# Kernel tuning notes

Hardware: AMD Instinct MI355X
Metric: run time of the kernel (lower is better)

Reference implementation:

```python
import jax, jax.numpy as jnp
import numpy as np

L, N, E, H, D, F = 2048, 2, 1024, 16, 64, 4096  # seq, batch, embed, heads, head_dim, ffn
EPS = 1e-5


def _ln(x, w, b):
    m = jnp.mean(x, axis=-1, keepdims=True)
    v = jnp.mean(jnp.square(x - m), axis=-1, keepdims=True)
    return (x - m) * jax.lax.rsqrt(v + EPS) * w + b


def setup_inputs() -> dict:
    key = jax.random.key(0)
    ks = jax.random.split(key, 16)
    s = 0.02
    f32 = jnp.float32
    return {
        "x": jax.random.normal(ks[0], (L, N, E), f32),
        "ln1_w": jnp.ones((E,), f32),
        "ln1_b": jnp.zeros((E,), f32),
        "wq": jax.random.normal(ks[1], (H * D, E), f32) * s,
        "bq": jnp.zeros((H * D,), f32),
        "wk": jax.random.normal(ks[2], (H * D, E), f32) * s,
        "bk": jnp.zeros((H * D,), f32),
        "wv": jax.random.normal(ks[3], (H * D, E), f32) * s,
        "bv": jnp.zeros((H * D,), f32),
        "wout": jax.random.normal(ks[4], (E, H * D), f32) * s,
        "bout": jnp.zeros((E,), f32),
        "ln2_w": jnp.ones((E,), f32),
        "ln2_b": jnp.zeros((E,), f32),
        "fc1_w": jax.random.normal(ks[5], (F, E), f32) * s,
        "fc1_b": jnp.zeros((F,), f32),
        "fc2_w": jax.random.normal(ks[6], (E, F), f32) * s,
        "fc2_b": jnp.zeros((E,), f32),
    }


def reference(x, ln1_w, ln1_b, wq, bq, wk, bk, wv, bv, wout, bout,
              ln2_w, ln2_b, fc1_w, fc1_b, fc2_w, fc2_b):
    scale = D ** (-0.5)
    residual = x
    h = _ln(x, ln1_w, ln1_b)                      # (L,N,E)
    q = (h @ wq.T + bq).reshape(L, N, H, D) * scale
    k = (h @ wk.T + bk).reshape(L, N, H, D)
    v = (h @ wv.T + bv).reshape(L, N, H, D)
    attn = jnp.einsum('qnhd,knhd->nhqk', q, k)    # (N,H,L,L) full score matrix
    causal = jnp.tril(jnp.ones((L, L), bool))
    attn = jnp.where(causal[None, None], attn, jnp.float32(-10000.0))
    p = jax.nn.softmax(attn, axis=-1)
    o = jnp.einsum('nhqk,knhd->qnhd', p, v).reshape(L, N, H * D)
    o = o @ wout.T + bout
    x = o + residual
    residual = x
    h = _ln(x, ln2_w, ln2_b)
    h = jax.nn.gelu(h @ fc1_w.T + fc1_b, approximate=False)
    h = h @ fc2_w.T + fc2_b
    return h + residual
```

## Files before the change

### kernel.cpp

```cpp
#include <hip/hip_runtime.h>
#include <hip/hip_bf16.h>
#include <math.h>

using bf16 = __hip_bfloat16;
typedef __bf16 bf16x8 __attribute__((ext_vector_type(8)));
typedef short  short4v __attribute__((ext_vector_type(4)));
typedef float  f32x4  __attribute__((ext_vector_type(4)));

static constexpr int Lq = 2048, Nb = 2, E = 1024, Hh = 16, Dd = 64, Ff = 4096;
static constexpr int MT = Lq * Nb;

__device__ __forceinline__ void async_lds16(const void* g, void* l) {
  __builtin_amdgcn_global_load_lds(
      (const __attribute__((address_space(1))) void*)g,
      (__attribute__((address_space(3))) void*)l, 16, 0, 0);
}
__device__ __forceinline__ bf16x8 ld8(const bf16* p) { return *(const bf16x8*)p; }
__device__ __forceinline__ short bfbits(float x) {
  bf16 t = __float2bfloat16(x);
  return *(short*)&t;
}
__device__ __forceinline__ float gelu_fast(float v) {
  const float y = fminf(2.302208f * (v + 0.044715f * v * v * v), 80.f);
  const float t = exp2f(y);
  return v * t / (t + 1.0f);
}

__global__ __launch_bounds__(256) void cvt_all_kernel(
    const float* __restrict__ wq, const float* __restrict__ wk,
    const float* __restrict__ wv, const float* __restrict__ wout,
    const float* __restrict__ fc1w, const float* __restrict__ fc2w,
    bf16* __restrict__ wqkvb, bf16* __restrict__ woutb,
    bf16* __restrict__ f1wb, bf16* __restrict__ f2wb) {
  const int i = blockIdx.x * 256 + threadIdx.x;
  const float* src;
  bf16* dst;
  size_t off;
  if (i < 786432) {
    const int r = i >> 18;
    off = (size_t)(i & 262143);
    src = (r == 0) ? wq : (r == 1) ? wk : wv;
    dst = wqkvb + (size_t)r * (E * E);
  } else if (i < 1048576) {
    off = (size_t)(i - 786432); src = wout; dst = woutb;
  } else if (i < 2097152) {
    off = (size_t)(i - 1048576); src = fc1w; dst = f1wb;
  } else {
    off = (size_t)(i - 2097152); src = fc2w; dst = f2wb;
  }
  float4 v = ((const float4*)src)[off];
  bf16 o4[4] = {__float2bfloat16(v.x), __float2bfloat16(v.y),
                __float2bfloat16(v.z), __float2bfloat16(v.w)};
  *(uint2*)(dst + 4 * off) = *(uint2*)o4;
}

template <int S, int H>
__device__ __forceinline__ void load_frags256(const char* Ab, const char* Bb,
                                              const int (&aoff)[8], const int (&boff)[4],
                                              bf16x8 (&a)[4], bf16x8 (&b)[4]) {
#pragma unroll
  for (int i = 0; i < 4; i++) a[i] = ld8((const bf16*)(Ab + S * 16384 + aoff[H * 4 + i]));
#pragma unroll
  for (int j = 0; j < 4; j++) b[j] = ld8((const bf16*)(Bb + S * 16384 + boff[j]));
}

template <int H>
__device__ __forceinline__ void mfma256(const bf16x8 (&a)[4], const bf16x8 (&b)[4],
                                        f32x4 (&acc)[8][4]) {
#pragma unroll
  for (int i = 0; i < 4; i++)
#pragma unroll
    for (int j = 0; j < 4; j++)
      acc[H * 4 + i][j] =
          __builtin_amdgcn_mfma_f32_16x16x32_bf16(a[i], b[j], acc[H * 4 + i][j], 0, 0, 0);
}

template <int K, int KSTR, int NOUT, int EPI>
__global__ __launch_bounds__(512, 2) void gemm256(
    const bf16* __restrict__ A, const bf16* __restrict__ W,
    const float* __restrict__ b1, const float* __restrict__ b2,
    const float* __restrict__ b3, float qscale,
    bf16* __restrict__ o0, bf16* __restrict__ o1,
    bf16* __restrict__ o2, bf16* __restrict__ o3) {
  extern __shared__ char smem[];
  constexpr int NKT = K / 64;
  static_assert(NKT >= 2, "need >=2 K-tiles");
  const int tid = threadIdx.x;
  const int w = tid >> 6, lane = tid & 63;
  const int quad = lane >> 4, l16 = lane & 15;
  const int wr = w >> 2, wc = w & 3;
  const int m0 = blockIdx.y * 256, n0 = blockIdx.x * 256;
  const int koff = blockIdx.z * K;

  const int o0b = tid << 4;
  const int o1b = o0b + 8192;
  const int r0 = o0b >> 6, r1 = o1b >> 6;
  const int c0 = ((((o0b >> 4) & 3) ^ ((o0b >> 7) & 3)) << 3);
  const int c1 = ((((o1b >> 4) & 3) ^ ((o1b >> 7) & 3)) << 3);
  const bf16* Ag0 = A + (size_t)(m0 + r0) * KSTR + koff + c0;
  const bf16* Ag1 = A + (size_t)(m0 + r1) * KSTR + koff + c1;
  const bf16* Wg0 = W + (size_t)(n0 + r0) * KSTR + koff + c0;
  const bf16* Wg1 = W + (size_t)(n0 + r1) * KSTR + koff + c1;
  const int ldsw = w << 10;

  int aoff[8], boff[4];
#pragma unroll
  for (int h = 0; h < 2; h++)
#pragma unroll
    for (int i = 0; i < 4; i++) {
      const int ra = wr * 128 + h * 64 + i * 16 + l16;
      aoff[h * 4 + i] = ra * 64 + ((quad ^ ((ra >> 1) & 3)) << 4);
    }
#pragma unroll
  for (int j = 0; j < 4; j++) {
    const int rb = wc * 64 + j * 16 + l16;
    boff[j] = rb * 64 + ((quad ^ ((rb >> 1) & 3)) << 4);
  }

  f32x4 acc[8][4];
#pragma unroll
  for (int i = 0; i < 8; i++)
#pragma unroll
    for (int j = 0; j < 4; j++)
#pragma unroll
      for (int r = 0; r < 4; r++) acc[i][j][r] = 0.f;

  {
    char* d = smem;
    async_lds16(Ag0, d + ldsw);
    async_lds16(Ag1, d + 8192 + ldsw);
    async_lds16(Wg0, d + 32768 + ldsw);
    async_lds16(Wg1, d + 32768 + 8192 + ldsw);
    async_lds16(Ag0 + 32, d + 16384 + ldsw);
    async_lds16(Ag1 + 32, d + 16384 + 8192 + ldsw);
    async_lds16(Wg0 + 32, d + 49152 + ldsw);
    async_lds16(Wg1 + 32, d + 49152 + 8192 + ldsw);
  }
  asm volatile("s_waitcnt vmcnt(4)" ::: "memory");
  __builtin_amdgcn_s_barrier();

  for (int kt = 0; kt < NKT; ++kt) {
    const char* Ab = smem + ((kt & 1) << 16);
    const char* Bb = Ab + 32768;
    char* Sd = smem + (((kt + 1) & 1) << 16);
    const int kn = (kt + 1) << 6;
    if (kt + 1 < NKT) {
      {
        bf16x8 a[4], b[4];
        load_frags256<0, 0>(Ab, Bb, aoff, boff, a, b);
        async_lds16(Ag0 + kn, Sd + ldsw);
        async_lds16(Ag1 + kn, Sd + 8192 + ldsw);
        __builtin_amdgcn_s_barrier();
        __builtin_amdgcn_s_setprio(1);
        mfma256<0>(a, b, acc);
        __builtin_amdgcn_s_setprio(0);
        __builtin_amdgcn_sched_barrier(0);
        __builtin_amdgcn_s_barrier();
      }
      {
        bf16x8 a[4], b[4];
        load_frags256<0, 1>(Ab, Bb, aoff, boff, a, b);
        async_lds16(Wg0 + kn, Sd + 32768 + ldsw);
        async_lds16(Wg1 + kn, Sd + 32768 + 8192 + ldsw);
        __builtin_amdgcn_s_barrier();
        __builtin_amdgcn_s_setprio(1);
        mfma256<1>(a, b, acc);
        __builtin_amdgcn_s_setprio(0);
        asm volatile("s_waitcnt vmcnt(4)" ::: "memory");
        __builtin_amdgcn_sched_barrier(0);
        __builtin_amdgcn_s_barrier();
      }
      {
        bf16x8 a[4], b[4];
        load_frags256<1, 0>(Ab, Bb, aoff, boff, a, b);
        async_lds16(Ag0 + kn + 32, Sd + 16384 + ldsw);
        async_lds16(Ag1 + kn + 32, Sd + 16384 + 8192 + ldsw);
        __builtin_amdgcn_s_barrier();
        __builtin_amdgcn_s_setprio(1);
        mfma256<0>(a, b, acc);
        __builtin_amdgcn_s_setprio(0);
        __builtin_amdgcn_sched_barrier(0);
        __builtin_amdgcn_s_barrier();
      }
      {
        bf16x8 a[4], b[4];
        load_frags256<1, 1>(Ab, Bb, aoff, boff, a, b);
        async_lds16(Wg0 + kn + 32, Sd + 49152 + ldsw);
        async_lds16(Wg1 + kn + 32, Sd + 49152 + 8192 + ldsw);
        __builtin_amdgcn_s_barrier();
        __builtin_amdgcn_s_setprio(1);
        mfma256<1>(a, b, acc);
        __builtin_amdgcn_s_setprio(0);
        asm volatile("s_waitcnt vmcnt(4)" ::: "memory");
        __builtin_amdgcn_sched_barrier(0);
        __builtin_amdgcn_s_barrier();
      }
    } else {
      {
        bf16x8 a[4], b[4];
        load_frags256<0, 0>(Ab, Bb, aoff, boff, a, b);
        __builtin_amdgcn_s_barrier();
        __builtin_amdgcn_s_setprio(1);
        mfma256<0>(a, b, acc);
        __builtin_amdgcn_s_setprio(0);
        __builtin_amdgcn_sched_barrier(0);
        __builtin_amdgcn_s_barrier();
      }
      {
        bf16x8 a[4], b[4];
        load_frags256<0, 1>(Ab, Bb, aoff, boff, a, b);
        __builtin_amdgcn_s_barrier();
        __builtin_amdgcn_s_setprio(1);
        mfma256<1>(a, b, acc);
        __builtin_amdgcn_s_setprio(0);
        asm volatile("s_waitcnt vmcnt(0)" ::: "memory");
        __builtin_amdgcn_sched_barrier(0);
        __builtin_amdgcn_s_barrier();
      }
      {
        bf16x8 a[4], b[4];
        load_frags256<1, 0>(Ab, Bb, aoff, boff, a, b);
        __builtin_amdgcn_s_barrier();
        __builtin_amdgcn_s_setprio(1);
        mfma256<0>(a, b, acc);
        __builtin_amdgcn_s_setprio(0);
        __builtin_amdgcn_sched_barrier(0);
        __builtin_amdgcn_s_barrier();
      }
      {
        bf16x8 a[4], b[4];
        load_frags256<1, 1>(Ab, Bb, aoff, boff, a, b);
        __builtin_amdgcn_s_barrier();
        __builtin_amdgcn_s_setprio(1);
        mfma256<1>(a, b, acc);
        __builtin_amdgcn_s_setprio(0);
      }
    }
  }

  if constexpr (EPI == 2) {
#pragma unroll
    for (int j = 0; j < 4; j++) {
      const int col = n0 + wc * 64 + j * 16 + l16;
      const float bv = b1[col];
#pragma unroll
      for (int mI = 0; mI < 8; mI++) {
        const int row = m0 + wr * 128 + mI * 16 + quad * 4;
#pragma unroll
        for (int r = 0; r < 4; r++) {
          o0[(size_t)(row + r) * NOUT + col] =
              __float2bfloat16(gelu_fast(acc[mI][j][r] + bv));
        }
      }
    }
  } else if constexpr (EPI == 3) {
    bf16* dst = (blockIdx.z == 0) ? o0
              : (blockIdx.z == 1) ? o1
              : (blockIdx.z == 2) ? o2 : o3;
#pragma unroll
    for (int j = 0; j < 4; j++) {
      const int col = n0 + wc * 64 + j * 16 + l16;
#pragma unroll
      for (int mI = 0; mI < 8; mI++) {
        const int row = m0 + wr * 128 + mI * 16 + quad * 4;
#pragma unroll
        for (int r = 0; r < 4; r++) {
          dst[(size_t)(row + r) * NOUT + col] = __float2bfloat16(acc[mI][j][r]);
        }
      }
    }
  } else {
    const int seg = n0 >> 10;
#pragma unroll
    for (int j = 0; j < 4; j++) {
      const int col = n0 + wc * 64 + j * 16 + l16;
      const float bv = (seg == 0) ? b1[col]
                     : (seg == 1) ? b2[col - 1024] : b3[col - 2048];
      const int d = col & 63;
#pragma unroll
      for (int mI = 0; mI < 8; mI++) {
        const int row = m0 + wr * 128 + mI * 16 + quad * 4;
#pragma unroll
        for (int r = 0; r < 4; r++) {
          const int tok = row + r, n = tok & 1, l = tok >> 1;
          float v = acc[mI][j][r] + bv;
          if (seg == 0) {
            o0[(size_t)tok * 1024 + col] = __float2bfloat16(v * qscale);
          } else if (seg == 1) {
            const int h = (col - 1024) >> 6, hh = n * 16 + h;
            o2[((((size_t)hh * 32 + (l >> 6)) * 8 + (d >> 3)) * 64 + (l & 63)) * 8 +
               (d & 7)] = __float2bfloat16(v);
          } else {
            const int h = (col - 2048) >> 6, hh = n * 16 + h;
            o1[((((size_t)hh * 32 + (l >> 6)) * 8 + ((l >> 3) & 7)) * 64 + d) * 8 +
               (l & 7)] = __float2bfloat16(v);
          }
        }
      }
    }
  }
}

__global__ __launch_bounds__(256) void reduce4_kernel(
    const bf16* __restrict__ P0, const bf16* __restrict__ P1,
    const bf16* __restrict__ P2, const bf16* __restrict__ P3,
    const float* __restrict__ bias, float* __restrict__ out) {
  const int i = blockIdx.x * 256 + threadIdx.x;
  const size_t e0 = (size_t)i * 4;
  const int col = (int)(e0 & (E - 1));
  uint2 a0 = *(const uint2*)(P0 + e0);
  uint2 a1 = *(const uint2*)(P1 + e0);
  uint2 a2 = *(const uint2*)(P2 + e0);
  uint2 a3 = *(const uint2*)(P3 + e0);
  const bf16* q0 = (const bf16*)&a0;
  const bf16* q1 = (const bf16*)&a1;
  const bf16* q2 = (const bf16*)&a2;
  const bf16* q3 = (const bf16*)&a3;
  float4 b = *(const float4*)(bias + col);
  float4 r = *(const float4*)(out + e0);
  float4 o;
  o.x = (float)q0[0] + (float)q1[0] + (float)q2[0] + (float)q3[0] + b.x + r.x;
  o.y = (float)q0[1] + (float)q1[1] + (float)q2[1] + (float)q3[1] + b.y + r.y;
  o.z = (float)q0[2] + (float)q1[2] + (float)q2[2] + (float)q3[2] + b.z + r.z;
  o.w = (float)q0[3] + (float)q1[3] + (float)q2[3] + (float)q3[3] + b.w + r.w;
  *(float4*)(out + e0) = o;
}

__global__ __launch_bounds__(256) void redln_kernel(
    const bf16* __restrict__ P, const float* __restrict__ bias,
    const float* __restrict__ res, const float* __restrict__ wgt,
    const float* __restrict__ bia, float* __restrict__ resout,
    bf16* __restrict__ h2) {
  const int t = blockIdx.x, tid = threadIdx.x;
  const size_t base = (size_t)t * E;
  const int e0 = tid * 4;
  uint2 u0 = *(const uint2*)(P + base + e0);
  uint2 u1 = *(const uint2*)(P + (size_t)MT * E + base + e0);
  const bf16* p0 = (const bf16*)&u0;
  const bf16* p1 = (const bf16*)&u1;
  float4 b = *(const float4*)(bias + e0);
  float4 r = *(const float4*)(res + base + e0);
  float v4[4];
  v4[0] = (float)p0[0] + (float)p1[0] + b.x + r.x;
  v4[1] = (float)p0[1] + (float)p1[1] + b.y + r.y;
  v4[2] = (float)p0[2] + (float)p1[2] + b.z + r.z;
  v4[3] = (float)p0[3] + (float)p1[3] + b.w + r.w;
  *(float4*)(resout + base + e0) = *(float4*)v4;

  float s = 0.f, ss = 0.f;
#pragma unroll
  for (int i = 0; i < 4; i++) { s += v4[i]; ss += v4[i] * v4[i]; }
  for (int off = 32; off > 0; off >>= 1) {
    s += __shfl_down(s, off, 64);
    ss += __shfl_down(ss, off, 64);
  }
  __shared__ float rs[4], rss[4], mv[2];
  const int w = tid >> 6;
  if ((tid & 63) == 0) { rs[w] = s; rss[w] = ss; }
  __syncthreads();
  if (tid == 0) {
    float S = rs[0] + rs[1] + rs[2] + rs[3];
    float SS = rss[0] + rss[1] + rss[2] + rss[3];
    float mean = S * (1.f / E);
    float var = SS * (1.f / E) - mean * mean;
    mv[0] = mean; mv[1] = rsqrtf(var + 1e-5f);
  }
  __syncthreads();
  const float mean = mv[0], rstd = mv[1];
  float4 wg = *(const float4*)(wgt + e0);
  float4 bb = *(const float4*)(bia + e0);
  bf16 o4[4];
  o4[0] = __float2bfloat16((v4[0] - mean) * rstd * wg.x + bb.x);
  o4[1] = __float2bfloat16((v4[1] - mean) * rstd * wg.y + bb.y);
  o4[2] = __float2bfloat16((v4[2] - mean) * rstd * wg.z + bb.z);
  o4[3] = __float2bfloat16((v4[3] - mean) * rstd * wg.w + bb.w);
  *(uint2*)(h2 + base + e0) = *(uint2*)o4;
}

__global__ __launch_bounds__(256) void ln_kernel(
    const float* __restrict__ x, const float* __restrict__ wgt,
    const float* __restrict__ bia, bf16* __restrict__ out) {
  const int t = blockIdx.x, tid = threadIdx.x;
  const size_t base = (size_t)t * E;
  float v4[4], s = 0.f, ss = 0.f;
#pragma unroll
  for (int i = 0; i < 4; i++) {
    float v = x[base + i * 256 + tid];
    v4[i] = v; s += v; ss += v * v;
  }
  for (int off = 32; off > 0; off >>= 1) {
    s += __shfl_down(s, off, 64);
    ss += __shfl_down(ss, off, 64);
  }
  __shared__ float rs[4], rss[4], mv[2];
  const int w = tid >> 6;
  if ((tid & 63) == 0) { rs[w] = s; rss[w] = ss; }
  __syncthreads();
  if (tid == 0) {
    float S = rs[0] + rs[1] + rs[2] + rs[3];
    float SS = rss[0] + rss[1] + rss[2] + rss[3];
    float mean = S * (1.f / E);
    float var = SS * (1.f / E) - mean * mean;
    mv[0] = mean; mv[1] = rsqrtf(var + 1e-5f);
  }
  __syncthreads();
  const float mean = mv[0], rstd = mv[1];
#pragma unroll
  for (int i = 0; i < 4; i++) {
    const int e = i * 256 + tid;
    float r = (v4[i] - mean) * rstd * wgt[e] + bia[e];
    out[base + e] = __float2bfloat16(r);
  }
}

__global__ __launch_bounds__(256) void attn_kernel(
    const bf16* __restrict__ Q1, const bf16* __restrict__ KT,
    const bf16* __restrict__ VT, bf16* __restrict__ O) {
  __shared__ __align__(16) bf16 KB[2][512 * 8];
  __shared__ __align__(16) bf16 VB[2][512 * 8];
  const int tid = threadIdx.x;
  const int w = tid >> 6, lane = tid & 63, quad = lane >> 4, l16 = lane & 15;
  const int bid = blockIdx.x;
  const int x = bid & 7;
  const int m = (bid >> 3) & 31;
  const int g = bid >> 8;
  const int j = m >> 2;
  const int hh = (m & 3) * 8 + x;
  const int qt = (g == 0) ? j : (g == 1) ? (31 - j) : (g == 2) ? (j + 8) : (23 - j);
  const int n = hh >> 4, h = hh & 15;

  const bf16* Qp = Q1 + n * E + h * Dd;
  const bf16* Kb = KT + (size_t)hh * 32 * 4096;
  const bf16* Vb = VT + (size_t)hh * 32 * 4096;
  const int so = w * 512 + lane * 8;

  const int ql = qt * 64 + w * 16 + l16;
  const bf16x8 aq0 = ld8(Qp + (size_t)ql * 2048 + quad * 8);
  const bf16x8 aq1 = ld8(Qp + (size_t)ql * 2048 + 32 + quad * 8);
  asm volatile("s_waitcnt vmcnt(0)" ::: "memory");

  async_lds16(Kb + so, &KB[0][w * 512]);
  async_lds16(Kb + 2048 + so, &KB[0][2048 + w * 512]);
  async_lds16(Vb + so, &VB[0][w * 512]);
  async_lds16(Vb + 2048 + so, &VB[0][2048 + w * 512]);

  f32x4 o_acc[4];
#pragma unroll
  for (int d = 0; d < 4; d++)
#pragma unroll
    for (int r = 0; r < 4; r++) o_acc[d][r] = 0.f;
  float m_run = -3e30f, l_run = 0.f;

  for (int kt = 0; kt <= qt; ++kt) {
    const bf16* KBb = KB[kt & 1];
    const bf16* VBb = VB[kt & 1];
    if (kt < qt) {
      const size_t tb = (size_t)(kt + 1) * 4096;
      bf16* Kd = &KB[(kt & 1) ^ 1][0];
      bf16* Vd = &VB[(kt & 1) ^ 1][0];
      async_lds16(Kb + tb + so, Kd + w * 512);
      async_lds16(Kb + tb + 2048 + so, Kd + 2048 + w * 512);
      async_lds16(Vb + tb + so, Vd + w * 512);
      async_lds16(Vb + tb + 2048 + so, Vd + 2048 + w * 512);
      asm volatile("s_waitcnt vmcnt(4)" ::: "memory");
    } else {
      asm volatile("s_waitcnt vmcnt(0)" ::: "memory");
    }
    __builtin_amdgcn_s_barrier();

    f32x4 s[4];
    __builtin_amdgcn_s_setprio(1);
#pragma unroll
    for (int ks = 0; ks < 4; ks++) {
      const bf16x8 kc0 = ld8(&KBb[(size_t)((quad)*64 + ks * 16 + l16) * 8]);
      const bf16x8 kc1 = ld8(&KBb[(size_t)((4 + quad) * 64 + ks * 16 + l16) * 8]);
#pragma unroll
      for (int r = 0; r < 4; r++) s[ks][r] = 0.f;
      s[ks] = __builtin_amdgcn_mfma_f32_16x16x32_bf16(kc0, aq0, s[ks], 0, 0, 0);
      s[ks] = __builtin_amdgcn_mfma_f32_16x16x32_bf16(kc1, aq1, s[ks], 0, 0, 0);
    }
    __builtin_amdgcn_s_setprio(0);

    if (kt == qt) {
#pragma unroll
      for (int ks = 0; ks < 4; ks++) {
#pragma unroll
        for (int r = 0; r < 4; r++) {
          const int kg = kt * 64 + ks * 16 + quad * 4 + r;
          if (kg > ql) s[ks][r] = -14427.0f;
        }
      }
    }

    float tmax = s[0][0];
#pragma unroll
    for (int ks = 0; ks < 4; ks++)
#pragma unroll
      for (int r = 0; r < 4; r++) tmax = fmaxf(tmax, s[ks][r]);
    tmax = fmaxf(tmax, __shfl_xor(tmax, 16, 64));
    tmax = fmaxf(tmax, __shfl_xor(tmax, 32, 64));
    float mbase = m_run;
    if (__any(tmax - m_run > 8.0f)) {
      const float mnew = fmaxf(m_run, tmax);
      const float alpha = exp2f(m_run - mnew);
      m_run = mnew;
      mbase = mnew;
      l_run *= alpha;
#pragma unroll
      for (int d = 0; d < 4; d++)
#pragma unroll
        for (int r = 0; r < 4; r++) o_acc[d][r] *= alpha;
    }
    float rsum = 0.f;
    short4v pf[4];
#pragma unroll
    for (int ks = 0; ks < 4; ks++) {
#pragma unroll
      for (int r = 0; r < 4; r++) {
        const float pv = exp2f(s[ks][r] - mbase);
        rsum += pv;
        pf[ks][r] = bfbits(pv);
      }
    }
    rsum += __shfl_xor(rsum, 16, 64);
    rsum += __shfl_xor(rsum, 32, 64);
    l_run += rsum;

    __builtin_amdgcn_s_setprio(1);
#pragma unroll
    for (int d = 0; d < 4; d++) {
#pragma unroll
      for (int ks = 0; ks < 4; ks++) {
        const int gg = ks * 2 + (quad >> 1);
        const short4v av =
            *(const short4v*)&VBb[(size_t)(gg * 64 + d * 16 + l16) * 8 + (quad & 1) * 4];
        o_acc[d] = __builtin_amdgcn_mfma_f32_16x16x16bf16_1k(av, pf[ks], o_acc[d], 0, 0, 0);
      }
    }
    __builtin_amdgcn_s_setprio(0);

    __builtin_amdgcn_sched_barrier(0);
    __builtin_amdgcn_s_barrier();
  }

  const float inv_l = 1.f / fmaxf(l_run, 1e-30f);
  const size_t obase = (size_t)ql * (Nb * E) + (size_t)n * E + h * Dd;
#pragma unroll
  for (int d = 0; d < 4; d++)
#pragma unroll
    for (int r = 0; r < 4; r++)
      O[obase + d * 16 + quad * 4 + r] = __float2bfloat16(o_acc[d][r] * inv_l);
}

extern "C" void kernel_launch(void* const* d_in, const int* in_sizes, int n_in,
                              void* d_out, int out_size, void* d_ws, size_t ws_size,
                              hipStream_t stream) {
  const float* x    = (const float*)d_in[0];
  const float* ln1w = (const float*)d_in[1];
  const float* ln1b = (const float*)d_in[2];
  const float* wq   = (const float*)d_in[3];
  const float* bq   = (const float*)d_in[4];
  const float* wk   = (const float*)d_in[5];
  const float* bk   = (const float*)d_in[6];
  const float* wv   = (const float*)d_in[7];
  const float* bv   = (const float*)d_in[8];
  const float* wout = (const float*)d_in[9];
  const float* bout = (const float*)d_in[10];
  const float* ln2w = (const float*)d_in[11];
  const float* ln2b = (const float*)d_in[12];
  const float* fc1w = (const float*)d_in[13];
  const float* fc1b = (const float*)d_in[14];
  const float* fc2w = (const float*)d_in[15];
  const float* fc2b = (const float*)d_in[16];

  char* ws = (char*)d_ws;
  bf16* wqkvb = (bf16*)(ws);
  bf16* woutb = (bf16*)(ws + ((size_t)6 << 20));
  bf16* f1wb  = (bf16*)(ws + ((size_t)8 << 20));
  bf16* f2wb  = (bf16*)(ws + ((size_t)16 << 20));
  bf16* h1    = (bf16*)(ws + ((size_t)24 << 20));
  bf16* qk1   = (bf16*)(ws + ((size_t)32 << 20));
  bf16* ktg   = (bf16*)(ws + ((size_t)40 << 20));
  bf16* vtg   = (bf16*)(ws + ((size_t)48 << 20));
  bf16* o     = (bf16*)(ws + ((size_t)56 << 20));
  bf16* Pout  = (bf16*)(ws + ((size_t)32 << 20));
  bf16* f1    = (bf16*)(ws + ((size_t)32 << 20));
  bf16* h2    = h1;
  bf16* FP0   = (bf16*)(ws);
  bf16* FP1   = (bf16*)(ws + ((size_t)8 << 20));
  bf16* FP2   = (bf16*)(ws + ((size_t)64 << 20));
  bf16* FP3   = (bf16*)(ws + ((size_t)72 << 20));
  float* outp = (float*)d_out;

  static bool g_shmem_attr = false;
  if (!g_shmem_attr) {
    hipFuncSetAttribute(reinterpret_cast<const void*>(gemm256<1024, 1024, 3072, 4>),
                        hipFuncAttributeMaxDynamicSharedMemorySize, 131072);
    hipFuncSetAttribute(reinterpret_cast<const void*>(gemm256<512, 1024, 1024, 3>),
                        hipFuncAttributeMaxDynamicSharedMemorySize, 131072);
    hipFuncSetAttribute(reinterpret_cast<const void*>(gemm256<1024, 1024, 4096, 2>),
                        hipFuncAttributeMaxDynamicSharedMemorySize, 131072);
    hipFuncSetAttribute(reinterpret_cast<const void*>(gemm256<1024, 4096, 1024, 3>),
                        hipFuncAttributeMaxDynamicSharedMemorySize, 131072);
    g_shmem_attr = true;
  }

  cvt_all_kernel<<<12288, 256, 0, stream>>>(wq, wk, wv, wout, fc1w, fc2w,
                                            wqkvb, woutb, f1wb, f2wb);

  ln_kernel<<<MT, 256, 0, stream>>>(x, ln1w, ln1b, h1);

  gemm256<1024, 1024, 3072, 4><<<dim3(12, 16), 512, 131072, stream>>>(
      h1, wqkvb, bq, bk, bv, 0.125f * 1.44269504f, qk1, vtg, ktg, nullptr);

  attn_kernel<<<1024, 256, 0, stream>>>(qk1, ktg, vtg, o);

  gemm256<512, 1024, 1024, 3><<<dim3(4, 16, 2), 512, 131072, stream>>>(
      o, woutb, nullptr, nullptr, nullptr, 1.f,
      Pout, Pout + (size_t)MT * E, nullptr, nullptr);
  redln_kernel<<<MT, 256, 0, stream>>>(Pout, bout, x, ln2w, ln2b, outp, h2);

  gemm256<1024, 1024, 4096, 2><<<dim3(Ff / 256, MT / 256), 512, 131072, stream>>>(
      h2, f1wb, fc1b, nullptr, nullptr, 1.f, f1, nullptr, nullptr, nullptr);

  gemm256<1024, 4096, 1024, 3><<<dim3(4, 16, 4), 512, 131072, stream>>>(
      f1, f2wb, nullptr, nullptr, nullptr, 1.f, FP0, FP1, FP2, FP3);
  reduce4_kernel<<<MT * E / 1024, 256, 0, stream>>>(FP0, FP1, FP2, FP3, fc2b, outp);
}
```

Measured before the change: 367.4 us.

## Replace 256x256 GEMM with smaller-tile high-occupancy 128x256 kernel

Swaps the hand-scheduled 256x256 GEMM, which used 128KB of dynamic LDS and 2 blocks per CU, for a 128x256 tile with K-step 32 and 48KB of static LDS, launch bounds raised to 4 blocks per CU. The aim is to hide latency through more resident waves and to double the grid size, replacing the fine-grained interleaved load/MFMA schedule. In exchange it gives up per-block reuse of loaded data and adds more barriers per unit of K, which may raise LDS and global traffic.

```diff
diff --git a/kernel.cpp b/kernel.cpp
--- a/kernel.cpp
+++ b/kernel.cpp
@@ -54,202 +54,89 @@
   *(uint2*)(dst + 4 * off) = *(uint2*)o4;
 }
 
-template <int S, int H>
-__device__ __forceinline__ void load_frags256(const char* Ab, const char* Bb,
-                                              const int (&aoff)[8], const int (&boff)[4],
-                                              bf16x8 (&a)[4], bf16x8 (&b)[4]) {
-#pragma unroll
-  for (int i = 0; i < 4; i++) a[i] = ld8((const bf16*)(Ab + S * 16384 + aoff[H * 4 + i]));
-#pragma unroll
-  for (int j = 0; j < 4; j++) b[j] = ld8((const bf16*)(Bb + S * 16384 + boff[j]));
-}
-
-template <int H>
-__device__ __forceinline__ void mfma256(const bf16x8 (&a)[4], const bf16x8 (&b)[4],
-                                        f32x4 (&acc)[8][4]) {
-#pragma unroll
-  for (int i = 0; i < 4; i++)
-#pragma unroll
-    for (int j = 0; j < 4; j++)
-      acc[H * 4 + i][j] =
-          __builtin_amdgcn_mfma_f32_16x16x32_bf16(a[i], b[j], acc[H * 4 + i][j], 0, 0, 0);
-}
-
 template <int K, int KSTR, int NOUT, int EPI>
-__global__ __launch_bounds__(512, 2) void gemm256(
+__global__ __launch_bounds__(512, 4) void gemm_tlp(
     const bf16* __restrict__ A, const bf16* __restrict__ W,
     const float* __restrict__ b1, const float* __restrict__ b2,
     const float* __restrict__ b3, float qscale,
     bf16* __restrict__ o0, bf16* __restrict__ o1,
     bf16* __restrict__ o2, bf16* __restrict__ o3) {
-  extern __shared__ char smem[];
-  constexpr int NKT = K / 64;
+  __shared__ __align__(16) bf16 sm[2][12288];
+  constexpr int NKT = K / 32;
   static_assert(NKT >= 2, "need >=2 K-tiles");
   const int tid = threadIdx.x;
   const int w = tid >> 6, lane = tid & 63;
   const int quad = lane >> 4, l16 = lane & 15;
-  const int wr = w >> 2, wc = w & 3;
-  const int m0 = blockIdx.y * 256, n0 = blockIdx.x * 256;
+  const int wm = (w >> 2) * 64, wn = (w & 3) * 64;
+  const int m0 = blockIdx.y * 128, n0 = blockIdx.x * 256;
   const int koff = blockIdx.z * K;
 
-  const int o0b = tid << 4;
-  const int o1b = o0b + 8192;
-  const int r0 = o0b >> 6, r1 = o1b >> 6;
-  const int c0 = ((((o0b >> 4) & 3) ^ ((o0b >> 7) & 3)) << 3);
-  const int c1 = ((((o1b >> 4) & 3) ^ ((o1b >> 7) & 3)) << 3);
-  const bf16* Ag0 = A + (size_t)(m0 + r0) * KSTR + koff + c0;
-  const bf16* Ag1 = A + (size_t)(m0 + r1) * KSTR + koff + c1;
-  const bf16* Wg0 = W + (size_t)(n0 + r0) * KSTR + koff + c0;
-  const bf16* Wg1 = W + (size_t)(n0 + r1) * KSTR + koff + c1;
-  const int ldsw = w << 10;
-
-  int aoff[8], boff[4];
-#pragma unroll
-  for (int h = 0; h < 2; h++)
-#pragma unroll
-    for (int i = 0; i < 4; i++) {
-      const int ra = wr * 128 + h * 64 + i * 16 + l16;
-      aoff[h * 4 + i] = ra * 64 + ((quad ^ ((ra >> 1) & 3)) << 4);
-    }
-#pragma unroll
-  for (int j = 0; j < 4; j++) {
-    const int rb = wc * 64 + j * 16 + l16;
-    boff[j] = rb * 64 + ((quad ^ ((rb >> 1) & 3)) << 4);
-  }
-
-  f32x4 acc[8][4];
-#pragma unroll
-  for (int i = 0; i < 8; i++)
+  const int srow = tid >> 2;
+  const int sca = ((tid & 3) ^ ((srow >> 1) & 3)) * 8;
+  const bf16* Asrc = A + (size_t)(m0 + srow) * KSTR + koff + sca;
+  const bf16* Wsrc0 = W + (size_t)(n0 + srow) * KSTR + koff + sca;
+  const bf16* Wsrc1 = W + (size_t)(n0 + 128 + srow) * KSTR + koff + sca;
+  const int d8 = tid * 8;
+
+  const int kq = ((quad ^ ((l16 >> 1) & 3)) << 3);
+
+  f32x4 acc[4][4];
+#pragma unroll
+  for (int i = 0; i < 4; i++)
 #pragma unroll
     for (int j = 0; j < 4; j++)
 #pragma unroll
       for (int r = 0; r < 4; r++) acc[i][j][r] = 0.f;
 
-  {
-    char* d = smem;
-    async_lds16(Ag0, d + ldsw);
-    async_lds16(Ag1, d + 8192 + ldsw);
-    async_lds16(Wg0, d + 32768 + ldsw);
-    async_lds16(Wg1, d + 32768 + 8192 + ldsw);
-    async_lds16(Ag0 + 32, d + 16384 + ldsw);
-    async_lds16(Ag1 + 32, d + 16384 + 8192 + ldsw);
-    async_lds16(Wg0 + 32, d + 49152 + ldsw);
-    async_lds16(Wg1 + 32, d + 49152 + 8192 + ldsw);
-  }
-  asm volatile("s_waitcnt vmcnt(4)" ::: "memory");
-  __builtin_amdgcn_s_barrier();
+  async_lds16(Asrc, &sm[0][d8]);
+  async_lds16(Wsrc0, &sm[0][4096 + d8]);
+  async_lds16(Wsrc1, &sm[0][8192 + d8]);
 
   for (int kt = 0; kt < NKT; ++kt) {
-    const char* Ab = smem + ((kt & 1) << 16);
-    const char* Bb = Ab + 32768;
-    char* Sd = smem + (((kt + 1) & 1) << 16);
-    const int kn = (kt + 1) << 6;
+    const bf16* S = sm[kt & 1];
     if (kt + 1 < NKT) {
-      {
-        bf16x8 a[4], b[4];
-        load_frags256<0, 0>(Ab, Bb, aoff, boff, a, b);
-        async_lds16(Ag0 + kn, Sd + ldsw);
-        async_lds16(Ag1 + kn, Sd + 8192 + ldsw);
-        __builtin_amdgcn_s_barrier();
-        __builtin_amdgcn_s_setprio(1);
-        mfma256<0>(a, b, acc);
-        __builtin_amdgcn_s_setprio(0);
-        __builtin_amdgcn_sched_barrier(0);
-        __builtin_amdgcn_s_barrier();
-      }
-      {
-        bf16x8 a[4], b[4];
-        load_frags256<0, 1>(Ab, Bb, aoff, boff, a, b);
-        async_lds16(Wg0 + kn, Sd + 32768 + ldsw);
-        async_lds16(Wg1 + kn, Sd + 32768 + 8192 + ldsw);
-        __builtin_amdgcn_s_barrier();
-        __builtin_amdgcn_s_setprio(1);
-        mfma256<1>(a, b, acc);
-        __builtin_amdgcn_s_setprio(0);
-        asm volatile("s_waitcnt vmcnt(4)" ::: "memory");
-        __builtin_amdgcn_sched_barrier(0);
-        __builtin_amdgcn_s_barrier();
-      }
-      {
-        bf16x8 a[4], b[4];
-        load_frags256<1, 0>(Ab, Bb, aoff, boff, a, b);
-        async_lds16(Ag0 + kn + 32, Sd + 16384 + ldsw);
-        async_lds16(Ag1 + kn + 32, Sd + 16384 + 8192 + ldsw);
-        __builtin_amdgcn_s_barrier();
-        __builtin_amdgcn_s_setprio(1);
-        mfma256<0>(a, b, acc);
-        __builtin_amdgcn_s_setprio(0);
-        __builtin_amdgcn_sched_barrier(0);
-        __builtin_amdgcn_s_barrier();
-      }
-      {
-        bf16x8 a[4], b[4];
-        load_frags256<1, 1>(Ab, Bb, aoff, boff, a, b);
-        async_lds16(Wg0 + kn + 32, Sd + 49152 + ldsw);
-        async_lds16(Wg1 + kn + 32, Sd + 49152 + 8192 + ldsw);
-        __builtin_amdgcn_s_barrier();
-        __builtin_amdgcn_s_setprio(1);
-        mfma256<1>(a, b, acc);
-        __builtin_amdgcn_s_setprio(0);
-        asm volatile("s_waitcnt vmcnt(4)" ::: "memory");
-        __builtin_amdgcn_sched_barrier(0);
-        __builtin_amdgcn_s_barrier();
-      }
+      const int kn = (kt + 1) * 32;
+      bf16* D = sm[(kt & 1) ^ 1];
+      async_lds16(Asrc + kn, &D[d8]);
+      async_lds16(Wsrc0 + kn, &D[4096 + d8]);
+      async_lds16(Wsrc1 + kn, &D[8192 + d8]);
+      asm volatile("s_waitcnt vmcnt(3)" ::: "memory");
     } else {
-      {
-        bf16x8 a[4], b[4];
-        load_frags256<0, 0>(Ab, Bb, aoff, boff, a, b);
-        __builtin_amdgcn_s_barrier();
-        __builtin_amdgcn_s_setprio(1);
-        mfma256<0>(a, b, acc);
-        __builtin_amdgcn_s_setprio(0);
-        __builtin_amdgcn_sched_barrier(0);
-        __builtin_amdgcn_s_barrier();
-      }
-      {
-        bf16x8 a[4], b[4];
-        load_frags256<0, 1>(Ab, Bb, aoff, boff, a, b);
-        __builtin_amdgcn_s_barrier();
-        __builtin_amdgcn_s_setprio(1);
-        mfma256<1>(a, b, acc);
-        __builtin_amdgcn_s_setprio(0);
-        asm volatile("s_waitcnt vmcnt(0)" ::: "memory");
-        __builtin_amdgcn_sched_barrier(0);
-        __builtin_amdgcn_s_barrier();
-      }
-      {
-        bf16x8 a[4], b[4];
-        load_frags256<1, 0>(Ab, Bb, aoff, boff, a, b);
-        __builtin_amdgcn_s_barrier();
-        __builtin_amdgcn_s_setprio(1);
-        mfma256<0>(a, b, acc);
-        __builtin_amdgcn_s_setprio(0);
-        __builtin_amdgcn_sched_barrier(0);
-        __builtin_amdgcn_s_barrier();
-      }
-      {
-        bf16x8 a[4], b[4];
-        load_frags256<1, 1>(Ab, Bb, aoff, boff, a, b);
-        __builtin_amdgcn_s_barrier();
-        __builtin_amdgcn_s_setprio(1);
-        mfma256<1>(a, b, acc);
-        __builtin_amdgcn_s_setprio(0);
-      }
-    }
+      asm volatile("s_waitcnt vmcnt(0)" ::: "memory");
+    }
+    __builtin_amdgcn_s_barrier();
+
+    bf16x8 a[4], b[4];
+#pragma unroll
+    for (int i = 0; i < 4; i++)
+      a[i] = ld8(&S[(wm + i * 16 + l16) * 32 + kq]);
+#pragma unroll
+    for (int j = 0; j < 4; j++)
+      b[j] = ld8(&S[4096 + (wn + j * 16 + l16) * 32 + kq]);
+
+    __builtin_amdgcn_s_setprio(1);
+#pragma unroll
+    for (int i = 0; i < 4; i++)
+#pragma unroll
+      for (int j = 0; j < 4; j++)
+        acc[i][j] = __builtin_amdgcn_mfma_f32_16x16x32_bf16(a[i], b[j], acc[i][j], 0, 0, 0);
+    __builtin_amdgcn_s_setprio(0);
+    __builtin_amdgcn_sched_barrier(0);
+    __builtin_amdgcn_s_barrier();
   }
 
   if constexpr (EPI == 2) {
 #pragma unroll
     for (int j = 0; j < 4; j++) {
-      const int col = n0 + wc * 64 + j * 16 + l16;
+      const int col = n0 + wn + j * 16 + l16;
       const float bv = b1[col];
 #pragma unroll
-      for (int mI = 0; mI < 8; mI++) {
-        const int row = m0 + wr * 128 + mI * 16 + quad * 4;
+      for (int i = 0; i < 4; i++) {
+        const int row = m0 + wm + i * 16 + quad * 4;
 #pragma unroll
         for (int r = 0; r < 4; r++) {
           o0[(size_t)(row + r) * NOUT + col] =
-              __float2bfloat16(gelu_fast(acc[mI][j][r] + bv));
+              __float2bfloat16(gelu_fast(acc[i][j][r] + bv));
         }
       }
     }
@@ -259,13 +146,13 @@
               : (blockIdx.z == 2) ? o2 : o3;
 #pragma unroll
     for (int j = 0; j < 4; j++) {
-      const int col = n0 + wc * 64 + j * 16 + l16;
-#pragma unroll
-      for (int mI = 0; mI < 8; mI++) {
-        const int row = m0 + wr * 128 + mI * 16 + quad * 4;
+      const int col = n0 + wn + j * 16 + l16;
+#pragma unroll
+      for (int i = 0; i < 4; i++) {
+        const int row = m0 + wm + i * 16 + quad * 4;
 #pragma unroll
         for (int r = 0; r < 4; r++) {
-          dst[(size_t)(row + r) * NOUT + col] = __float2bfloat16(acc[mI][j][r]);
+          dst[(size_t)(row + r) * NOUT + col] = __float2bfloat16(acc[i][j][r]);
         }
       }
     }
@@ -273,17 +160,17 @@
     const int seg = n0 >> 10;
 #pragma unroll
     for (int j = 0; j < 4; j++) {
-      const int col = n0 + wc * 64 + j * 16 + l16;
+      const int col = n0 + wn + j * 16 + l16;
       const float bv = (seg == 0) ? b1[col]
                      : (seg == 1) ? b2[col - 1024] : b3[col - 2048];
       const int d = col & 63;
 #pragma unroll
-      for (int mI = 0; mI < 8; mI++) {
-        const int row = m0 + wr * 128 + mI * 16 + quad * 4;
+      for (int i = 0; i < 4; i++) {
+        const int row = m0 + wm + i * 16 + quad * 4;
 #pragma unroll
         for (int r = 0; r < 4; r++) {
           const int tok = row + r, n = tok & 1, l = tok >> 1;
-          float v = acc[mI][j][r] + bv;
+          float v = acc[i][j][r] + bv;
           if (seg == 0) {
             o0[(size_t)tok * 1024 + col] = __float2bfloat16(v * qscale);
           } else if (seg == 1) {
@@ -592,38 +479,25 @@
   bf16* FP3   = (bf16*)(ws + ((size_t)72 << 20));
   float* outp = (float*)d_out;
 
-  static bool g_shmem_attr = false;
-  if (!g_shmem_attr) {
-    hipFuncSetAttribute(reinterpret_cast<const void*>(gemm256<1024, 1024, 3072, 4>),
-                        hipFuncAttributeMaxDynamicSharedMemorySize, 131072);
-    hipFuncSetAttribute(reinterpret_cast<const void*>(gemm256<512, 1024, 1024, 3>),
-                        hipFuncAttributeMaxDynamicSharedMemorySize, 131072);
-    hipFuncSetAttribute(reinterpret_cast<const void*>(gemm256<1024, 1024, 4096, 2>),
-                        hipFuncAttributeMaxDynamicSharedMemorySize, 131072);
-    hipFuncSetAttribute(reinterpret_cast<const void*>(gemm256<1024, 4096, 1024, 3>),
-                        hipFuncAttributeMaxDynamicSharedMemorySize, 131072);
-    g_shmem_attr = true;
-  }
-
   cvt_all_kernel<<<12288, 256, 0, stream>>>(wq, wk, wv, wout, fc1w, fc2w,
                                             wqkvb, woutb, f1wb, f2wb);
 
   ln_kernel<<<MT, 256, 0, stream>>>(x, ln1w, ln1b, h1);
 
-  gemm256<1024, 1024, 3072, 4><<<dim3(12, 16), 512, 131072, stream>>>(
+  gemm_tlp<1024, 1024, 3072, 4><<<dim3(12, 32), 512, 0, stream>>>(
       h1, wqkvb, bq, bk, bv, 0.125f * 1.44269504f, qk1, vtg, ktg, nullptr);
 
   attn_kernel<<<1024, 256, 0, stream>>>(qk1, ktg, vtg, o);
 
-  gemm256<512, 1024, 1024, 3><<<dim3(4, 16, 2), 512, 131072, stream>>>(
+  gemm_tlp<512, 1024, 1024, 3><<<dim3(4, 32, 2), 512, 0, stream>>>(
       o, woutb, nullptr, nullptr, nullptr, 1.f,
       Pout, Pout + (size_t)MT * E, nullptr, nullptr);
   redln_kernel<<<MT, 256, 0, stream>>>(Pout, bout, x, ln2w, ln2b, outp, h2);
 
-  gemm256<1024, 1024, 4096, 2><<<dim3(Ff / 256, MT / 256), 512, 131072, stream>>>(
+  gemm_tlp<1024, 1024, 4096, 2><<<dim3(16, 32), 512, 0, stream>>>(
       h2, f1wb, fc1b, nullptr, nullptr, 1.f, f1, nullptr, nullptr, nullptr);
 
-  gemm256<1024, 4096, 1024, 3><<<dim3(4, 16, 4), 512, 131072, stream>>>(
+  gemm_tlp<1024, 4096, 1024, 3><<<dim3(4, 32, 4), 512, 0, stream>>>(
       f1, f2wb, nullptr, nullptr, nullptr, 1.f, FP0, FP1, FP2, FP3);
   reduce4_kernel<<<MT * E / 1024, 256, 0, stream>>>(FP0, FP1, FP2, FP3, fc2b, outp);
 }
```

After: 345.0 us. 6.1% less time.
